# Optimization experiments

Measured on AMD Instinct MI355X. Metric: run time of the kernel, lower is better.

The kernel has to match this reference:

```python
import jax, jax.numpy as jnp
import numpy as np

T, N, E = 4, 20000, 640000
D_IN, D_OUT = 256, 128
RRELU_SLOPE = (1.0 / 8.0 + 1.0 / 3.0) / 2.0  # RReLU eval-mode slope


def setup_inputs() -> dict:
    key = jax.random.key(0)
    ks = jax.random.split(key, 16)

    def glorot(k, shape):
        lim = np.sqrt(6.0 / (shape[0] + shape[1]))
        return jax.random.uniform(k, shape, jnp.float32, -lim, lim)

    node_embs = jax.random.normal(ks[0], (T, N, D_IN), jnp.float32)
    edge_index = jax.random.randint(ks[1], (T, 2, E), 0, N, jnp.int32)
    edge_weight = jax.random.uniform(ks[2], (T, E), jnp.float32)
    mask = jnp.zeros((T, N), jnp.float32)
    return {
        "node_embs": node_embs,
        "edge_index": edge_index,
        "edge_weight": edge_weight,
        "mask": mask,
        "p": glorot(ks[3], (D_IN, 1)),
        "Wz": glorot(ks[4], (D_IN, D_IN)),
        "Uz": glorot(ks[5], (D_IN, D_IN)),
        "bz": jnp.zeros((D_IN, D_OUT), jnp.float32),
        "Wr": glorot(ks[6], (D_IN, D_IN)),
        "Ur": glorot(ks[7], (D_IN, D_IN)),
        "br": jnp.zeros((D_IN, D_OUT), jnp.float32),
        "Wh": glorot(ks[8], (D_IN, D_IN)),
        "Uh": glorot(ks[9], (D_IN, D_IN)),
        "bh": jnp.zeros((D_IN, D_OUT), jnp.float32),
        "W0": glorot(ks[10], (D_IN, D_OUT)),
    }


def reference(node_embs, edge_index, edge_weight, mask, p, Wz, Uz, bz, Wr, Ur, br, Wh, Uh, bh, W0):
    n = node_embs.shape[1]
    k = W0.shape[1]

    def step(W, inputs):
        x, ei, w, m = inputs  # x: [N, D_IN]
        # --- TopK summary (EvolveGCN-H) ---
        scores = (x @ p)[:, 0] / jnp.linalg.norm(p) + m  # [N]
        vals, idx = jax.lax.top_k(scores, k)
        xt = (x[idx] * jnp.tanh(vals)[:, None]).T  # [D_IN, k]
        # --- matrix GRU cell: hidden state is the GCN weight W ---
        z = jax.nn.sigmoid(Wz @ xt + Uz @ W + bz)
        r = jax.nn.sigmoid(Wr @ xt + Ur @ W + br)
        h = jnp.tanh(Wh @ xt + Uh @ (r * W) + bh)
        Wn = (1.0 - z) * W + z * h  # [D_IN, D_OUT]
        # --- sparse GCN conv: adj @ (x @ Wn) ---
        y = x @ Wn  # [N, D_OUT]
        dst, src = ei[0], ei[1]
        agg = jax.ops.segment_sum(w[:, None] * y[src], dst, num_segments=n)
        out = jnp.where(agg >= 0, agg, RRELU_SLOPE * agg)
        return Wn, out

    _, out_seq = jax.lax.scan(step, W0, (node_embs, edge_index, edge_weight, mask))
    return out_seq  # [T, N, D_OUT]
```

## Files before the change

### kernel.cpp

```cpp
#include <hip/hip_runtime.h>

typedef unsigned short u16;
typedef unsigned int u32;
typedef unsigned long long u64;

#define T_ 4
#define N_ 20000
#define E_ 640000
#define DIN 256
#define DOUT 128
#define NT (T_*N_)
#define TE (T_*E_)
#define SLOPE 0.22916666666666666f

#define NB 125
#define BNODES 160
#define CAP 5632
#define NBTOT (T_*NB)

#define SGRAN 11
#define NSB 10
#define NBIN (32*5*NSB)
#define NBIN_PAD 2048
#define BOSTRIDE 168

typedef __attribute__((ext_vector_type(8))) short short8;
typedef __attribute__((ext_vector_type(4))) float f32x4;

__device__ __forceinline__ float blo(u32 u) { return __uint_as_float(u << 16); }
__device__ __forceinline__ float bhi(u32 u) { return __uint_as_float(u & 0xFFFF0000u); }
__device__ __forceinline__ u16 f2bf(float f) {
    u32 u = __float_as_uint(f);
    return (u16)((u + 0x7FFFu + ((u >> 16) & 1u)) >> 16);
}
__device__ __forceinline__ u32 fkey(float f) {
    u32 u = __float_as_uint(f);
    return (u & 0x80000000u) ? ~u : (u | 0x80000000u);
}
__device__ __forceinline__ float fkeyinv(u32 k) {
    u32 u = (k & 0x80000000u) ? (k ^ 0x80000000u) : ~k;
    return __uint_as_float(u);
}

__global__ __launch_bounds__(256) void k_scores(const float* x, const float* p, const float* mask,
                                                float* scores, u16* xb16,
                                                const float* Wz, const float* Uz, const float* Wr,
                                                const float* Ur, const float* Wh, const float* Uh,
                                                u32* Tp) {
    int tid = threadIdx.x;
    if (blockIdx.x >= 5000) {
        int bid = blockIdx.x - 5000;
        int m = bid >> 7, b = bid & 127;
        int idx = b * 256 + tid;
        int d2 = idx & 127, i = idx >> 7;
        const float* src;
        switch (m) {
            case 0: src = Wz; break;
            case 1: src = Uz; break;
            case 2: src = Wr; break;
            case 3: src = Ur; break;
            case 4: src = Wh; break;
            default: src = Uh; break;
        }
        float lo = src[i * 256 + 2 * d2];
        float hi = src[i * 256 + 2 * d2 + 1];
        Tp[m * 32768 + d2 * 256 + i] = (u32)f2bf(lo) | ((u32)f2bf(hi) << 16);
        return;
    }
    __shared__ float pl[256];
    __shared__ float s_invn;
    pl[tid] = p[tid];
    __syncthreads();
    if (tid < 64) {
        float v = pl[tid] * pl[tid] + pl[tid + 64] * pl[tid + 64] +
                  pl[tid + 128] * pl[tid + 128] + pl[tid + 192] * pl[tid + 192];
        for (int o = 32; o > 0; o >>= 1) v += __shfl_xor(v, o);
        if (tid == 0) s_invn = 1.0f / sqrtf(v);
    }
    __syncthreads();
    int wid = tid >> 6, lane = tid & 63;
    for (int it = 0; it < 4; ++it) {
        int node = blockIdx.x * 16 + wid * 4 + it;
        const float* row = x + (size_t)node * DIN + lane * 4;
        float4 u = *(const float4*)row;
        float d = u.x * pl[lane * 4 + 0] + u.y * pl[lane * 4 + 1] +
                  u.z * pl[lane * 4 + 2] + u.w * pl[lane * 4 + 3];
        u32 p0 = (u32)f2bf(u.x) | ((u32)f2bf(u.y) << 16);
        u32 p1 = (u32)f2bf(u.z) | ((u32)f2bf(u.w) << 16);
        *(uint2*)(xb16 + (size_t)node * DIN + lane * 4) = make_uint2(p0, p1);
        for (int o = 32; o > 0; o >>= 1) d += __shfl_xor(d, o);
        if (lane == 0) scores[node] = d * s_invn + mask[node];
    }
}

__global__ __launch_bounds__(256) void k_bin(const int* ei, const float* ew,
                                             int* gcur, uint2* binned) {
    int blk = blockIdx.x;
    int t = blk / 250, ci = blk - t * 250;
    int ebase = ci * 2560;
    int tid = threadIdx.x;
    __shared__ u32 hist[128], sc[128], gbase[128];
    __shared__ uint2 stage[2560];
    if (tid < 128) hist[tid] = 0;
    __syncthreads();
    u32 px[10]; u32 pw[10]; u16 rk[10];
#pragma unroll
    for (int k = 0; k < 10; ++k) {
        int e = ebase + tid + k * 256;
        int dst = ei[t * (2 * E_) + e];
        int src = ei[t * (2 * E_) + E_ + e];
        float w = ew[t * E_ + e];
        int b = dst / BNODES;
        int dl = dst - b * BNODES;
        px[k] = (u32)(t * N_ + src) | ((u32)dl << 17) | ((u32)b << 25);
        pw[k] = __float_as_uint(w);
        rk[k] = (u16)atomicAdd(&hist[b], 1u);
    }
    __syncthreads();
    if (tid < 128) sc[tid] = hist[tid];
    __syncthreads();
    for (int o = 1; o < 128; o <<= 1) {
        u32 v = 0;
        if (tid < 128) { v = sc[tid]; if (tid >= o) v += sc[tid - o]; }
        __syncthreads();
        if (tid < 128) sc[tid] = v;
        __syncthreads();
    }
    if (tid < NB) gbase[tid] = (u32)atomicAdd(&gcur[t * NB + tid], (int)hist[tid]);
#pragma unroll
    for (int k = 0; k < 10; ++k) {
        int b = px[k] >> 25;
        u32 slot = (sc[b] - hist[b]) + rk[k];
        stage[slot] = make_uint2(px[k], pw[k]);
    }
    __syncthreads();
    for (int s = tid; s < 2560; s += 256) {
        uint2 v = stage[s];
        int b = v.x >> 25;
        u32 local = gbase[b] + ((u32)s - (sc[b] - hist[b]));
        if (local < CAP)
            binned[(size_t)(t * NB + b) * CAP + local] = v;
    }
}

__global__ __launch_bounds__(512) void k_scatter(const int* gcur, uint2* binned, int* bandoff,
                                                 const float* scores, const float* x, float* xtT) {
    int bg = blockIdx.x;
    int tid = threadIdx.x;
    if (bg >= NBTOT) {
        int t = bg - NBTOT;
        const float* sc = scores + t * N_;
        __shared__ u32 hist[256];
        __shared__ u32 sh_dig, sh_need;
        __shared__ u64 sel[256];
        __shared__ u32 selCount;
        __shared__ u32 idxl[128];
        __shared__ float tvl[128];
        u32 kreg[40];
#pragma unroll
        for (int p = 0; p < 40; ++p) {
            int i = tid + p * 512;
            kreg[p] = (i < N_) ? fkey(sc[i]) : 0u;
        }
        u32 pref = 0;
        u32 need = 128;
        for (int pass = 0; pass < 4; ++pass) {
            int shift = 24 - 8 * pass;
            if (tid < 256) hist[tid] = 0;
            __syncthreads();
#pragma unroll
            for (int p = 0; p < 40; ++p) {
                int i = tid + p * 512;
                u32 k = kreg[p];
                bool ok = (i < N_) && ((pass == 0) || ((k >> (shift + 8)) == pref));
                if (ok) atomicAdd(&hist[(k >> shift) & 255u], 1u);
            }
            __syncthreads();
            if (tid < 64) {
                int l = tid;
                u32 s = hist[4 * l] + hist[4 * l + 1] + hist[4 * l + 2] + hist[4 * l + 3];
                u32 S = s;
                for (int o = 1; o < 64; o <<= 1) {
                    u32 y = __shfl_down(S, o);
                    if (l + o < 64) S += y;
                }
                u64 m = __ballot(S >= need);
                int L = 63 - __builtin_clzll(m);
                if (l == L) {
                    u32 Snext = S - s;
                    u32 r = 0;
                    for (int dd = 3; dd >= 0; --dd) {
                        u32 hb = hist[4 * L + dd];
                        r += hb;
                        if (Snext + r >= need) {
                            sh_dig = (u32)(4 * L + dd);
                            sh_need = need - (Snext + r - hb);
                            break;
                        }
                    }
                }
            }
            __syncthreads();
            pref = (pref << 8) | sh_dig;
            need = sh_need;
            __syncthreads();
        }
        if (tid == 0) selCount = 0;
        __syncthreads();
        u32 theta = pref;
#pragma unroll
        for (int p = 0; p < 40; ++p) {
            int i = tid + p * 512;
            u32 k = kreg[p];
            if (i < N_ && k >= theta) {
                u32 pos = atomicAdd(&selCount, 1u);
                if (pos < 256) sel[pos] = (((u64)(k ^ 0xFFFFFFFFu)) << 32) | (u32)i;
            }
        }
        __syncthreads();
        u32 c = selCount;
        if (c > 256) c = 256;
        if (tid < 256 && (u32)tid >= c) sel[tid] = 0xFFFFFFFFFFFFFFFFull;
        __syncthreads();
        for (int k2 = 2; k2 <= 256; k2 <<= 1) {
            for (int jj = k2 >> 1; jj > 0; jj >>= 1) {
                if (tid < 256) {
                    int i = tid, ixj = i ^ jj;
                    if (ixj > i) {
                        u64 A = sel[i], B = sel[ixj];
                        bool asc = ((i & k2) == 0);
                        bool sw = asc ? (A > B) : (A < B);
                        if (sw) { sel[i] = B; sel[ixj] = A; }
                    }
                }
                __syncthreads();
            }
        }
        if (tid < 128) {
            u64 v = sel[tid];
            u32 k = ((u32)(v >> 32)) ^ 0xFFFFFFFFu;
            idxl[tid] = (u32)(v & 0xFFFFFFFFu);
            tvl[tid] = tanhf(fkeyinv(k));
        }
        __syncthreads();
        float* xt_t = xtT + t * (DIN * DOUT);
        const float* xb = x + (size_t)t * N_ * DIN;
        for (int e2 = tid; e2 < DIN * DOUT; e2 += 512) {
            int j = e2 >> 8, d = e2 & 255;
            xt_t[e2] = xb[(size_t)idxl[j] * DIN + d] * tvl[j];
        }
        return;
    }
    int t = bg / NB;
    uint2* bucket = binned + (size_t)bg * CAP;
    int cnt = gcur[bg]; if (cnt > CAP) cnt = CAP;
    int tbase = t * N_;
    __shared__ u32 nhist[NBIN_PAD];
    __shared__ u32 binstart[NBIN_PAD];
    __shared__ u32 wsum[8];
    for (int i = tid; i < NBIN_PAD; i += 512) nhist[i] = 0;
    __syncthreads();
    u32 vx[11]; u32 vw[11]; u16 r_[11]; u16 bn_[11];
#pragma unroll
    for (int k = 0; k < 11; ++k) {
        int e = tid + k * 512;
        uint2 v;
        if (e < cnt) {
            v = bucket[e];
        } else {
            v = make_uint2(((u32)(e % BNODES) << 17) | (u32)(tbase + N_ - 1), 0u);
        }
        vx[k] = v.x; vw[k] = v.y;
        int dl = (v.x >> 17) & 255;
        int s = (int)(v.x & 0x1FFFFu) - tbase;
        int bin = (dl / 5) * (5 * NSB) + (dl % 5) * NSB + (s >> SGRAN);
        bn_[k] = (u16)bin;
        r_[k] = (u16)atomicAdd(&nhist[bin], 1u);
    }
    __syncthreads();
    u32 loc1, loc2, loc3, tsum;
    {
        int b0 = tid * 4;
        u32 a = nhist[b0], b = nhist[b0 + 1], c = nhist[b0 + 2], d = nhist[b0 + 3];
        loc1 = a; loc2 = a + b; loc3 = a + b + c; tsum = a + b + c + d;
    }
    int lane = tid & 63, wv = tid >> 6;
    u32 xsc = tsum;
    for (int o = 1; o < 64; o <<= 1) { u32 yv = __shfl_up(xsc, o); if (lane >= o) xsc += yv; }
    if (lane == 63) wsum[wv] = xsc;
    __syncthreads();
    u32 wpre = 0;
    for (int wq = 0; wq < wv; ++wq) wpre += wsum[wq];
    u32 tpre = wpre + xsc - tsum;
    {
        int b0 = tid * 4;
        binstart[b0] = tpre;
        binstart[b0 + 1] = tpre + loc1;
        binstart[b0 + 2] = tpre + loc2;
        binstart[b0 + 3] = tpre + loc3;
    }
    __syncthreads();
    if (tid < 161) {
        int v = (tid < 160) ? (int)binstart[tid * NSB] : CAP;
        bandoff[bg * BOSTRIDE + tid] = v;
    }
#pragma unroll
    for (int k = 0; k < 11; ++k) {
        u32 pos = binstart[bn_[k]] + r_[k];
        bucket[pos] = make_uint2(vx[k] & 0x1FFFFFFu, vw[k]);
    }
}

__global__ __launch_bounds__(1024) void k_gru(const float* xtT, const float* W0, const u32* Tp,
                                              const float* bz, const float* br, const float* bh,
                                              u16* WnT) {
    int j = blockIdx.x;
    int tid = threadIdx.x;
    int i = tid & 255;
    int qk = tid >> 8;
    __shared__ float sxt[256], sW[256], srw[256];
    __shared__ float p1[4][256], p2[4][256];
    const u32* WzT = Tp;
    const u32* UzT = Tp + 32768;
    const u32* WrT = Tp + 65536;
    const u32* UrT = Tp + 98304;
    const u32* WhT = Tp + 131072;
    const u32* UhT = Tp + 163840;
    float wv = W0[i * 128 + j];
    float azb = bz[i * 128 + j];
    float arb = br[i * 128 + j];
    float ahb = bh[i * 128 + j];
    int d2base = qk * 32;
    for (int t = 0; t < T_; ++t) {
        __syncthreads();
        if (qk == 0) {
            sxt[i] = xtT[t * 32768 + j * 256 + i];
            sW[i] = wv;
        }
        __syncthreads();
        float az = 0.f, ar = 0.f;
#pragma unroll 4
        for (int dd = 0; dd < 32; ++dd) {
            int d2 = d2base + dd;
            float x0 = sxt[2 * d2], x1 = sxt[2 * d2 + 1];
            float w0 = sW[2 * d2], w1 = sW[2 * d2 + 1];
            u32 a = WzT[d2 * 256 + i], b = UzT[d2 * 256 + i];
            u32 cc = WrT[d2 * 256 + i], dv = UrT[d2 * 256 + i];
            az += blo(a) * x0 + bhi(a) * x1 + blo(b) * w0 + bhi(b) * w1;
            ar += blo(cc) * x0 + bhi(cc) * x1 + blo(dv) * w0 + bhi(dv) * w1;
        }
        p1[qk][i] = az;
        p2[qk][i] = ar;
        __syncthreads();
        float azs = p1[0][i] + p1[1][i] + p1[2][i] + p1[3][i] + azb;
        float ars = p2[0][i] + p2[1][i] + p2[2][i] + p2[3][i] + arb;
        float z = 1.0f / (1.0f + expf(-azs));
        float r = 1.0f / (1.0f + expf(-ars));
        if (qk == 0) srw[i] = r * wv;
        __syncthreads();
        float ah = 0.f;
#pragma unroll 4
        for (int dd = 0; dd < 32; ++dd) {
            int d2 = d2base + dd;
            float x0 = sxt[2 * d2], x1 = sxt[2 * d2 + 1];
            float r0 = srw[2 * d2], r1 = srw[2 * d2 + 1];
            u32 a = WhT[d2 * 256 + i], b = UhT[d2 * 256 + i];
            ah += blo(a) * x0 + bhi(a) * x1 + blo(b) * r0 + bhi(b) * r1;
        }
        p1[qk][i] = ah;
        __syncthreads();
        float ahs = p1[0][i] + p1[1][i] + p1[2][i] + p1[3][i] + ahb;
        float hh = tanhf(ahs);
        float wn = (1.0f - z) * wv + z * hh;
        if (qk == 0) WnT[t * 32768 + j * 256 + i] = f2bf(wn);
        wv = wn;
    }
}

__global__ __launch_bounds__(128) void k_gemm(const u16* xb16, const u16* WnT, u16* y) {
    int t = blockIdx.y;
    const u16* xb = xb16 + (size_t)t * N_ * DIN;
    const u16* Bt = WnT + t * (DIN * DOUT);
    u16* yb = y + (size_t)t * N_ * DOUT;
    int wid = threadIdx.x >> 6, lane = threadIdx.x & 63;
    int quad = lane >> 4, lm = lane & 15;
    int rowBase = blockIdx.x * 64 + wid * 32;
    f32x4 acc[2][8];
#pragma unroll
    for (int mi = 0; mi < 2; ++mi)
#pragma unroll
        for (int ni = 0; ni < 8; ++ni) acc[mi][ni] = (f32x4){0.f, 0.f, 0.f, 0.f};
    size_t aoff[2];
#pragma unroll
    for (int mi = 0; mi < 2; ++mi) {
        int r = rowBase + mi * 16 + lm;
        if (r > N_ - 1) r = N_ - 1;
        aoff[mi] = (size_t)r * DIN + quad * 8;
    }
    const u16* bbase = Bt + lm * 256 + quad * 8;
    for (int kk = 0; kk < 256; kk += 32) {
        short8 a0 = *(const short8*)(xb + aoff[0] + kk);
        short8 a1 = *(const short8*)(xb + aoff[1] + kk);
#pragma unroll
        for (int ni = 0; ni < 8; ++ni) {
            short8 b = *(const short8*)(bbase + ni * 4096 + kk);
            acc[0][ni] = __builtin_amdgcn_mfma_f32_16x16x32_bf16(a0, b, acc[0][ni], 0, 0, 0);
            acc[1][ni] = __builtin_amdgcn_mfma_f32_16x16x32_bf16(a1, b, acc[1][ni], 0, 0, 0);
        }
    }
#pragma unroll
    for (int mi = 0; mi < 2; ++mi)
#pragma unroll
        for (int ni = 0; ni < 8; ++ni)
#pragma unroll
            for (int r = 0; r < 4; ++r) {
                int row = rowBase + mi * 16 + quad * 4 + r;
                if (row < N_) yb[(size_t)row * DOUT + ni * 16 + lm] = f2bf(acc[mi][ni][r]);
            }
}

__global__ __launch_bounds__(512, 4) void k_agg(const uint2* binned, const int* bandoff,
                                                const u16* y, float* out) {
    int bid = blockIdx.x;
    int xcd = bid & 7;
    int t = xcd >> 1;
    int bl = ((bid >> 3) << 1) + (xcd & 1);
    if (bl >= NB) return;
    int bg = t * NB + bl;
    const uint2* bucket = binned + (size_t)bg * CAP;
    const int* bo = bandoff + bg * BOSTRIDE;
    int w = threadIdx.x >> 6, lane = threadIdx.x & 63;
    int q = lane >> 4, lq = lane & 15;
    int Q = (w << 2) | q;
    __shared__ float acc[BNODES][DOUT];
    const u16* yq = y + lq * 8;

#define FMA8(mm, vv)                                                    \
    {                                                                   \
        float wt = __uint_as_float(mm.y);                               \
        a0 += wt * blo(vv.x); a1 += wt * bhi(vv.x);                     \
        a2 += wt * blo(vv.y); a3 += wt * bhi(vv.y);                     \
        a4 += wt * blo(vv.z); a5 += wt * bhi(vv.z);                     \
        a6 += wt * blo(vv.w); a7 += wt * bhi(vv.w);                     \
    }

#pragma unroll
    for (int d = 0; d < 5; ++d) {
        int e = bo[Q * 5 + d];
        int eend = bo[Q * 5 + d + 1];
        float a0 = 0.f, a1 = 0.f, a2 = 0.f, a3 = 0.f;
        float a4 = 0.f, a5 = 0.f, a6 = 0.f, a7 = 0.f;
        for (; e + 8 <= eend; e += 8) {
            uint2 m0 = bucket[e];
            uint2 m1 = bucket[e + 1];
            uint2 m2 = bucket[e + 2];
            uint2 m3 = bucket[e + 3];
            uint2 m4 = bucket[e + 4];
            uint2 m5 = bucket[e + 5];
            uint2 m6 = bucket[e + 6];
            uint2 m7 = bucket[e + 7];
            uint4 v0 = *(const uint4*)(yq + (size_t)(m0.x & 0x1FFFFu) * DOUT);
            uint4 v1 = *(const uint4*)(yq + (size_t)(m1.x & 0x1FFFFu) * DOUT);
            uint4 v2 = *(const uint4*)(yq + (size_t)(m2.x & 0x1FFFFu) * DOUT);
            uint4 v3 = *(const uint4*)(yq + (size_t)(m3.x & 0x1FFFFu) * DOUT);
            uint4 v4 = *(const uint4*)(yq + (size_t)(m4.x & 0x1FFFFu) * DOUT);
            uint4 v5 = *(const uint4*)(yq + (size_t)(m5.x & 0x1FFFFu) * DOUT);
            uint4 v6 = *(const uint4*)(yq + (size_t)(m6.x & 0x1FFFFu) * DOUT);
            uint4 v7 = *(const uint4*)(yq + (size_t)(m7.x & 0x1FFFFu) * DOUT);
            FMA8(m0, v0)
            FMA8(m1, v1)
            FMA8(m2, v2)
            FMA8(m3, v3)
            FMA8(m4, v4)
            FMA8(m5, v5)
            FMA8(m6, v6)
            FMA8(m7, v7)
        }
        for (; e < eend; ++e) {
            uint2 m = bucket[e];
            uint4 v = *(const uint4*)(yq + (size_t)(m.x & 0x1FFFFu) * DOUT);
            FMA8(m, v)
        }
        float4* rp = (float4*)&acc[Q * 5 + d][lq * 8];
        rp[0] = make_float4(a0, a1, a2, a3);
        rp[1] = make_float4(a4, a5, a6, a7);
    }
#undef FMA8
    int gbase = t * N_ + bl * BNODES + w * 20;
#pragma unroll
    for (int r = 0; r < 20; ++r) {
        float v0 = acc[w * 20 + r][2 * lane], v1 = acc[w * 20 + r][2 * lane + 1];
        v0 = (v0 >= 0.f) ? v0 : SLOPE * v0;
        v1 = (v1 >= 0.f) ? v1 : SLOPE * v1;
        *(float2*)(out + (size_t)(gbase + r) * DOUT + 2 * lane) = make_float2(v0, v1);
    }
}

extern "C" void kernel_launch(void* const* d_in, const int* in_sizes, int n_in,
                              void* d_out, int out_size, void* d_ws, size_t ws_size,
                              hipStream_t stream) {
    const float* x = (const float*)d_in[0];
    const int* ei = (const int*)d_in[1];
    const float* ew = (const float*)d_in[2];
    const float* mask = (const float*)d_in[3];
    const float* p = (const float*)d_in[4];
    const float* Wz = (const float*)d_in[5];
    const float* Uz = (const float*)d_in[6];
    const float* bz = (const float*)d_in[7];
    const float* Wr = (const float*)d_in[8];
    const float* Ur = (const float*)d_in[9];
    const float* br = (const float*)d_in[10];
    const float* Wh = (const float*)d_in[11];
    const float* Uh = (const float*)d_in[12];
    const float* bh = (const float*)d_in[13];
    const float* W0 = (const float*)d_in[14];
    float* out = (float*)d_out;

    char* w = (char*)d_ws;
    u16* xb16 = (u16*)w;        w += (size_t)NT * DIN * 2;
    float* scores = (float*)w;  w += 320256;
    float* xtT = (float*)w;     w += 4 * 32768 * 4;
    u16* WnT = (u16*)w;         w += 4 * 32768 * 2;
    u32* Tp = (u32*)w;          w += 6 * 32768 * 4;
    u16* y = (u16*)w;           w += (size_t)NT * DOUT * 2;
    uint2* binned = (uint2*)w;  w += (size_t)NBTOT * CAP * 8;
    int* gcur = (int*)w;        w += 2048;
    int* bandoff = (int*)w;     w += NBTOT * BOSTRIDE * 4;

    hipMemsetAsync(gcur, 0, 2048, stream);

    k_scores<<<5768, 256, 0, stream>>>(x, p, mask, scores, xb16, Wz, Uz, Wr, Ur, Wh, Uh, Tp);
    k_bin<<<1000, 256, 0, stream>>>(ei, ew, gcur, binned);
    k_scatter<<<NBTOT + 4, 512, 0, stream>>>(gcur, binned, bandoff, scores, x, xtT);
    k_gru<<<128, 1024, 0, stream>>>(xtT, W0, Tp, bz, br, bh, WnT);
    k_gemm<<<dim3(313, 4), 128, 0, stream>>>(xb16, WnT, y);
    k_agg<<<512, 512, 0, stream>>>(binned, bandoff, y, out);
}
```

Before: 380.6 us.

## Reorder edge bins by source band across destinations and keep accumulators in registers

```diff
diff --git a/kernel.cpp b/kernel.cpp
--- a/kernel.cpp
+++ b/kernel.cpp
@@ -20,9 +20,9 @@
 
 #define SGRAN 11
 #define NSB 10
-#define NBIN (32*5*NSB)
+#define NBIN (32*NSB*5)
 #define NBIN_PAD 2048
-#define BOSTRIDE 168
+#define BOSTRIDE 1608
 
 typedef __attribute__((ext_vector_type(8))) short short8;
 typedef __attribute__((ext_vector_type(4))) float f32x4;
@@ -273,7 +273,7 @@
         vx[k] = v.x; vw[k] = v.y;
         int dl = (v.x >> 17) & 255;
         int s = (int)(v.x & 0x1FFFFu) - tbase;
-        int bin = (dl / 5) * (5 * NSB) + (dl % 5) * NSB + (s >> SGRAN);
+        int bin = (dl / 5) * (NSB * 5) + (s >> SGRAN) * 5 + (dl % 5);
         bn_[k] = (u16)bin;
         r_[k] = (u16)atomicAdd(&nhist[bin], 1u);
     }
@@ -300,9 +300,9 @@
         binstart[b0 + 3] = tpre + loc3;
     }
     __syncthreads();
-    if (tid < 161) {
-        int v = (tid < 160) ? (int)binstart[tid * NSB] : CAP;
-        bandoff[bg * BOSTRIDE + tid] = v;
+    for (int i = tid; i < NBIN + 1; i += 512) {
+        int v = (i < NBIN) ? (int)binstart[i] : CAP;
+        bandoff[bg * BOSTRIDE + i] = v;
     }
 #pragma unroll
     for (int k = 0; k < 11; ++k) {
@@ -432,67 +432,67 @@
     int w = threadIdx.x >> 6, lane = threadIdx.x & 63;
     int q = lane >> 4, lq = lane & 15;
     int Q = (w << 2) | q;
-    __shared__ float acc[BNODES][DOUT];
     const u16* yq = y + lq * 8;
 
-#define FMA8(mm, vv)                                                    \
-    {                                                                   \
-        float wt = __uint_as_float(mm.y);                               \
-        a0 += wt * blo(vv.x); a1 += wt * bhi(vv.x);                     \
-        a2 += wt * blo(vv.y); a3 += wt * bhi(vv.y);                     \
-        a4 += wt * blo(vv.z); a5 += wt * bhi(vv.z);                     \
-        a6 += wt * blo(vv.w); a7 += wt * bhi(vv.w);                     \
-    }
-
+    float a0[5], a1[5], a2[5], a3[5], a4[5], a5[5], a6[5], a7[5];
 #pragma unroll
     for (int d = 0; d < 5; ++d) {
-        int e = bo[Q * 5 + d];
-        int eend = bo[Q * 5 + d + 1];
-        float a0 = 0.f, a1 = 0.f, a2 = 0.f, a3 = 0.f;
-        float a4 = 0.f, a5 = 0.f, a6 = 0.f, a7 = 0.f;
-        for (; e + 8 <= eend; e += 8) {
-            uint2 m0 = bucket[e];
-            uint2 m1 = bucket[e + 1];
-            uint2 m2 = bucket[e + 2];
-            uint2 m3 = bucket[e + 3];
-            uint2 m4 = bucket[e + 4];
-            uint2 m5 = bucket[e + 5];
-            uint2 m6 = bucket[e + 6];
-            uint2 m7 = bucket[e + 7];
-            uint4 v0 = *(const uint4*)(yq + (size_t)(m0.x & 0x1FFFFu) * DOUT);
-            uint4 v1 = *(const uint4*)(yq + (size_t)(m1.x & 0x1FFFFu) * DOUT);
-            uint4 v2 = *(const uint4*)(yq + (size_t)(m2.x & 0x1FFFFu) * DOUT);
-            uint4 v3 = *(const uint4*)(yq + (size_t)(m3.x & 0x1FFFFu) * DOUT);
-            uint4 v4 = *(const uint4*)(yq + (size_t)(m4.x & 0x1FFFFu) * DOUT);
-            uint4 v5 = *(const uint4*)(yq + (size_t)(m5.x & 0x1FFFFu) * DOUT);
-            uint4 v6 = *(const uint4*)(yq + (size_t)(m6.x & 0x1FFFFu) * DOUT);
-            uint4 v7 = *(const uint4*)(yq + (size_t)(m7.x & 0x1FFFFu) * DOUT);
-            FMA8(m0, v0)
-            FMA8(m1, v1)
-            FMA8(m2, v2)
-            FMA8(m3, v3)
-            FMA8(m4, v4)
-            FMA8(m5, v5)
-            FMA8(m6, v6)
-            FMA8(m7, v7)
-        }
-        for (; e < eend; ++e) {
-            uint2 m = bucket[e];
-            uint4 v = *(const uint4*)(yq + (size_t)(m.x & 0x1FFFFu) * DOUT);
-            FMA8(m, v)
-        }
-        float4* rp = (float4*)&acc[Q * 5 + d][lq * 8];
-        rp[0] = make_float4(a0, a1, a2, a3);
-        rp[1] = make_float4(a4, a5, a6, a7);
+        a0[d] = 0.f; a1[d] = 0.f; a2[d] = 0.f; a3[d] = 0.f;
+        a4[d] = 0.f; a5[d] = 0.f; a6[d] = 0.f; a7[d] = 0.f;
+    }
+
+#define FMA8(dd, mm, vv)                                                  \
+    {                                                                     \
+        float wt = __uint_as_float(mm.y);                                 \
+        a0[dd] += wt * blo(vv.x); a1[dd] += wt * bhi(vv.x);               \
+        a2[dd] += wt * blo(vv.y); a3[dd] += wt * bhi(vv.y);               \
+        a4[dd] += wt * blo(vv.z); a5[dd] += wt * bhi(vv.z);               \
+        a6[dd] += wt * blo(vv.w); a7[dd] += wt * bhi(vv.w);               \
+    }
+
+    int e = bo[Q * 50];
+    for (int b = 0; b < NSB; ++b) {
+#pragma unroll
+        for (int d = 0; d < 5; ++d) {
+            int eend = bo[Q * 50 + b * 5 + d + 1];
+            for (; e + 4 <= eend; e += 4) {
+                uint2 m0 = bucket[e];
+                uint2 m1 = bucket[e + 1];
+                uint2 m2 = bucket[e + 2];
+                uint2 m3 = bucket[e + 3];
+                uint4 v0 = *(const uint4*)(yq + (size_t)(m0.x & 0x1FFFFu) * DOUT);
+                uint4 v1 = *(const uint4*)(yq + (size_t)(m1.x & 0x1FFFFu) * DOUT);
+                uint4 v2 = *(const uint4*)(yq + (size_t)(m2.x & 0x1FFFFu) * DOUT);
+                uint4 v3 = *(const uint4*)(yq + (size_t)(m3.x & 0x1FFFFu) * DOUT);
+                FMA8(d, m0, v0)
+                FMA8(d, m1, v1)
+                FMA8(d, m2, v2)
+                FMA8(d, m3, v3)
+            }
+            for (; e < eend; ++e) {
+                uint2 m = bucket[e];
+                uint4 v = *(const uint4*)(yq + (size_t)(m.x & 0x1FFFFu) * DOUT);
+                FMA8(d, m, v)
+            }
+        }
     }
 #undef FMA8
-    int gbase = t * N_ + bl * BNODES + w * 20;
-#pragma unroll
-    for (int r = 0; r < 20; ++r) {
-        float v0 = acc[w * 20 + r][2 * lane], v1 = acc[w * 20 + r][2 * lane + 1];
-        v0 = (v0 >= 0.f) ? v0 : SLOPE * v0;
-        v1 = (v1 >= 0.f) ? v1 : SLOPE * v1;
-        *(float2*)(out + (size_t)(gbase + r) * DOUT + 2 * lane) = make_float2(v0, v1);
+    int growbase = t * N_ + bl * BNODES + Q * 5;
+#pragma unroll
+    for (int d = 0; d < 5; ++d) {
+        float r0 = a0[d], r1 = a1[d], r2 = a2[d], r3 = a3[d];
+        float r4 = a4[d], r5 = a5[d], r6 = a6[d], r7 = a7[d];
+        r0 = (r0 >= 0.f) ? r0 : SLOPE * r0;
+        r1 = (r1 >= 0.f) ? r1 : SLOPE * r1;
+        r2 = (r2 >= 0.f) ? r2 : SLOPE * r2;
+        r3 = (r3 >= 0.f) ? r3 : SLOPE * r3;
+        r4 = (r4 >= 0.f) ? r4 : SLOPE * r4;
+        r5 = (r5 >= 0.f) ? r5 : SLOPE * r5;
+        r6 = (r6 >= 0.f) ? r6 : SLOPE * r6;
+        r7 = (r7 >= 0.f) ? r7 : SLOPE * r7;
+        float* ob = out + (size_t)(growbase + d) * DOUT + lq * 8;
+        *(float4*)ob = make_float4(r0, r1, r2, r3);
+        *(float4*)(ob + 4) = make_float4(r4, r5, r6, r7);
     }
 }
 
@@ -525,7 +525,7 @@
     u16* y = (u16*)w;           w += (size_t)NT * DOUT * 2;
     uint2* binned = (uint2*)w;  w += (size_t)NBTOT * CAP * 8;
     int* gcur = (int*)w;        w += 2048;
-    int* bandoff = (int*)w;     w += NBTOT * BOSTRIDE * 4;
+    int* bandoff = (int*)w;     w += (size_t)NBTOT * BOSTRIDE * 4;
 
     hipMemsetAsync(gcur, 0, 2048, stream);
 
```

After: 448.1 us. 1.18x slower.

## Reorder edge bins by source band and accumulate into shared-memory rows directly

Applied to the files above, without the earlier changes.

```diff
diff --git a/kernel.cpp b/kernel.cpp
--- a/kernel.cpp
+++ b/kernel.cpp
@@ -20,9 +20,9 @@
 
 #define SGRAN 11
 #define NSB 10
-#define NBIN (32*5*NSB)
+#define NBIN (32*NSB*5)
 #define NBIN_PAD 2048
-#define BOSTRIDE 168
+#define BOSTRIDE 40
 
 typedef __attribute__((ext_vector_type(8))) short short8;
 typedef __attribute__((ext_vector_type(4))) float f32x4;
@@ -273,7 +273,7 @@
         vx[k] = v.x; vw[k] = v.y;
         int dl = (v.x >> 17) & 255;
         int s = (int)(v.x & 0x1FFFFu) - tbase;
-        int bin = (dl / 5) * (5 * NSB) + (dl % 5) * NSB + (s >> SGRAN);
+        int bin = (dl / 5) * (NSB * 5) + (s >> SGRAN) * 5 + (dl % 5);
         bn_[k] = (u16)bin;
         r_[k] = (u16)atomicAdd(&nhist[bin], 1u);
     }
@@ -300,8 +300,8 @@
         binstart[b0 + 3] = tpre + loc3;
     }
     __syncthreads();
-    if (tid < 161) {
-        int v = (tid < 160) ? (int)binstart[tid * NSB] : CAP;
+    if (tid < 33) {
+        int v = (tid < 32) ? (int)binstart[tid * (NSB * 5)] : CAP;
         bandoff[bg * BOSTRIDE + tid] = v;
     }
 #pragma unroll
@@ -433,59 +433,58 @@
     int q = lane >> 4, lq = lane & 15;
     int Q = (w << 2) | q;
     __shared__ float acc[BNODES][DOUT];
+#pragma unroll
+    for (int r = 0; r < 20; ++r)
+        *(float2*)&acc[w * 20 + r][2 * lane] = make_float2(0.f, 0.f);
     const u16* yq = y + lq * 8;
-
-#define FMA8(mm, vv)                                                    \
+    int e = bo[Q];
+    int eend = bo[Q + 1];
+
+#define RMW(mm, vv)                                                     \
     {                                                                   \
+        int dl = (int)((mm.x >> 17) & 255u);                            \
         float wt = __uint_as_float(mm.y);                               \
-        a0 += wt * blo(vv.x); a1 += wt * bhi(vv.x);                     \
-        a2 += wt * blo(vv.y); a3 += wt * bhi(vv.y);                     \
-        a4 += wt * blo(vv.z); a5 += wt * bhi(vv.z);                     \
-        a6 += wt * blo(vv.w); a7 += wt * bhi(vv.w);                     \
-    }
-
-#pragma unroll
-    for (int d = 0; d < 5; ++d) {
-        int e = bo[Q * 5 + d];
-        int eend = bo[Q * 5 + d + 1];
-        float a0 = 0.f, a1 = 0.f, a2 = 0.f, a3 = 0.f;
-        float a4 = 0.f, a5 = 0.f, a6 = 0.f, a7 = 0.f;
-        for (; e + 8 <= eend; e += 8) {
-            uint2 m0 = bucket[e];
-            uint2 m1 = bucket[e + 1];
-            uint2 m2 = bucket[e + 2];
-            uint2 m3 = bucket[e + 3];
-            uint2 m4 = bucket[e + 4];
-            uint2 m5 = bucket[e + 5];
-            uint2 m6 = bucket[e + 6];
-            uint2 m7 = bucket[e + 7];
-            uint4 v0 = *(const uint4*)(yq + (size_t)(m0.x & 0x1FFFFu) * DOUT);
-            uint4 v1 = *(const uint4*)(yq + (size_t)(m1.x & 0x1FFFFu) * DOUT);
-            uint4 v2 = *(const uint4*)(yq + (size_t)(m2.x & 0x1FFFFu) * DOUT);
-            uint4 v3 = *(const uint4*)(yq + (size_t)(m3.x & 0x1FFFFu) * DOUT);
-            uint4 v4 = *(const uint4*)(yq + (size_t)(m4.x & 0x1FFFFu) * DOUT);
-            uint4 v5 = *(const uint4*)(yq + (size_t)(m5.x & 0x1FFFFu) * DOUT);
-            uint4 v6 = *(const uint4*)(yq + (size_t)(m6.x & 0x1FFFFu) * DOUT);
-            uint4 v7 = *(const uint4*)(yq + (size_t)(m7.x & 0x1FFFFu) * DOUT);
-            FMA8(m0, v0)
-            FMA8(m1, v1)
-            FMA8(m2, v2)
-            FMA8(m3, v3)
-            FMA8(m4, v4)
-            FMA8(m5, v5)
-            FMA8(m6, v6)
-            FMA8(m7, v7)
-        }
-        for (; e < eend; ++e) {
-            uint2 m = bucket[e];
-            uint4 v = *(const uint4*)(yq + (size_t)(m.x & 0x1FFFFu) * DOUT);
-            FMA8(m, v)
-        }
-        float4* rp = (float4*)&acc[Q * 5 + d][lq * 8];
-        rp[0] = make_float4(a0, a1, a2, a3);
-        rp[1] = make_float4(a4, a5, a6, a7);
-    }
-#undef FMA8
+        float4* rp = (float4*)&acc[dl][lq * 8];                         \
+        float4 r0 = rp[0], r1 = rp[1];                                  \
+        r0.x += wt * blo(vv.x); r0.y += wt * bhi(vv.x);                 \
+        r0.z += wt * blo(vv.y); r0.w += wt * bhi(vv.y);                 \
+        r1.x += wt * blo(vv.z); r1.y += wt * bhi(vv.z);                 \
+        r1.z += wt * blo(vv.w); r1.w += wt * bhi(vv.w);                 \
+        rp[0] = r0; rp[1] = r1;                                         \
+    }
+
+    for (; e + 8 <= eend; e += 8) {
+        uint2 m0 = bucket[e];
+        uint2 m1 = bucket[e + 1];
+        uint2 m2 = bucket[e + 2];
+        uint2 m3 = bucket[e + 3];
+        uint2 m4 = bucket[e + 4];
+        uint2 m5 = bucket[e + 5];
+        uint2 m6 = bucket[e + 6];
+        uint2 m7 = bucket[e + 7];
+        uint4 v0 = *(const uint4*)(yq + (size_t)(m0.x & 0x1FFFFu) * DOUT);
+        uint4 v1 = *(const uint4*)(yq + (size_t)(m1.x & 0x1FFFFu) * DOUT);
+        uint4 v2 = *(const uint4*)(yq + (size_t)(m2.x & 0x1FFFFu) * DOUT);
+        uint4 v3 = *(const uint4*)(yq + (size_t)(m3.x & 0x1FFFFu) * DOUT);
+        uint4 v4 = *(const uint4*)(yq + (size_t)(m4.x & 0x1FFFFu) * DOUT);
+        uint4 v5 = *(const uint4*)(yq + (size_t)(m5.x & 0x1FFFFu) * DOUT);
+        uint4 v6 = *(const uint4*)(yq + (size_t)(m6.x & 0x1FFFFu) * DOUT);
+        uint4 v7 = *(const uint4*)(yq + (size_t)(m7.x & 0x1FFFFu) * DOUT);
+        RMW(m0, v0)
+        RMW(m1, v1)
+        RMW(m2, v2)
+        RMW(m3, v3)
+        RMW(m4, v4)
+        RMW(m5, v5)
+        RMW(m6, v6)
+        RMW(m7, v7)
+    }
+    for (; e < eend; ++e) {
+        uint2 m = bucket[e];
+        uint4 v = *(const uint4*)(yq + (size_t)(m.x & 0x1FFFFu) * DOUT);
+        RMW(m, v)
+    }
+#undef RMW
     int gbase = t * N_ + bl * BNODES + w * 20;
 #pragma unroll
     for (int r = 0; r < 20; ++r) {
```

Measured after the change: 395.5 us. +3.9%, slower.
